# Optimization experiments

Measured on AMD Instinct MI355X. Metric: run time of the kernel, lower is better.

Reference implementation:

```python
import jax, jax.numpy as jnp
import numpy as np

EMBED_DIM = 1024
NUM_HEADS = 16
HEAD_DIM = EMBED_DIM // NUM_HEADS
B, S = 4, 2048


def setup_inputs() -> dict:
    key = jax.random.key(0)
    k1, k2, k3 = jax.random.split(key, 3)
    scale = 1.0 / np.sqrt(EMBED_DIM)
    x = jax.random.normal(k1, (B, S, EMBED_DIM), dtype=jnp.float32)
    W_qkv = jax.random.normal(k2, (EMBED_DIM, 3 * EMBED_DIM), dtype=jnp.float32) * scale
    b_qkv = jnp.zeros((3 * EMBED_DIM,), dtype=jnp.float32)
    W_out = jax.random.normal(k3, (EMBED_DIM, EMBED_DIM), dtype=jnp.float32) * scale
    b_out = jnp.zeros((EMBED_DIM,), dtype=jnp.float32)
    return {"x": x, "W_qkv": W_qkv, "b_qkv": b_qkv, "W_out": W_out, "b_out": b_out}


def reference(x, W_qkv, b_qkv, W_out, b_out):
    b, s, e = x.shape
    # fused QKV projection -> [b, s, 3, h, d]
    qkv = (x @ W_qkv + b_qkv).reshape(b, s, 3, NUM_HEADS, HEAD_DIM)
    qkv = jnp.transpose(qkv, (2, 0, 3, 1, 4))  # [3, b, h, s, d]
    q, k, v = qkv[0], qkv[1], qkv[2]
    scale = HEAD_DIM ** 0.5
    scores = jnp.einsum('bhqd,bhkd->bhqk', q, k) / scale  # [b, h, s, s]
    weights = jax.nn.softmax(scores, axis=-1)
    ctx = jnp.einsum('bhqk,bhkd->bhqd', weights, v)  # [b, h, s, d]
    ctx = jnp.transpose(ctx, (0, 2, 1, 3)).reshape(b, s, e)
    return ctx @ W_out + b_out
```

## Files before the change

### kernel.cpp

```cpp
#include <hip/hip_runtime.h>
#include <math.h>

#define B_ 4
#define S_ 2048
#define E_ 1024
#define H_ 16
#define D_ 64
#define M_TOT 8192
#define N_QKV 3072
#define K_ 1024

typedef __attribute__((ext_vector_type(8))) __bf16 bf16x8;
typedef __attribute__((ext_vector_type(2))) __bf16 bf16x2;
typedef __attribute__((ext_vector_type(8))) unsigned short u16x8;
typedef __attribute__((ext_vector_type(16))) float f32x16;

static __device__ __forceinline__ float bf2f(unsigned short u) {
  union { unsigned int u; float f; } x; x.u = ((unsigned int)u) << 16;
  return x.f;
}
static __device__ __forceinline__ unsigned int pack_bf16(float lo, float hi) {
  bf16x2 t; t[0] = (__bf16)lo; t[1] = (__bf16)hi;
  return __builtin_bit_cast(unsigned int, t);
}
static __device__ __forceinline__ void perm32swap(unsigned int& a, unsigned int& b) {
  asm volatile("v_permlane32_swap_b32 %0, %1" : "+v"(a), "+v"(b));
}

static __device__ __forceinline__ void gload16(const void* g, void* l) {
  __builtin_amdgcn_global_load_lds(
      (const __attribute__((address_space(1))) void*)g,
      (__attribute__((address_space(3))) void*)l, 16, 0, 0);
}

__global__ __launch_bounds__(256) void cvt_k(const float* __restrict__ in,
                                             unsigned short* __restrict__ out,
                                             int n8) {
  int i = blockIdx.x * 256 + threadIdx.x;
  if (i >= n8) return;
  float4 a = *reinterpret_cast<const float4*>(in + (size_t)i * 8);
  float4 b = *reinterpret_cast<const float4*>(in + (size_t)i * 8 + 4);
  uint4 o;
  o.x = pack_bf16(a.x, a.y); o.y = pack_bf16(a.z, a.w);
  o.z = pack_bf16(b.x, b.y); o.w = pack_bf16(b.z, b.w);
  *reinterpret_cast<uint4*>(out + (size_t)i * 8) = o;
}

__global__ __launch_bounds__(256) void tcvt_k(const float* __restrict__ in,
                                              unsigned short* __restrict__ out,
                                              int K, int N) {
  __shared__ float t[64][65];
  int n0 = blockIdx.x * 64, k0 = blockIdx.y * 64;
  int r = threadIdx.x >> 4, c = (threadIdx.x & 15) * 4;
#pragma unroll
  for (int it = 0; it < 4; ++it) {
    float4 v = *reinterpret_cast<const float4*>(&in[(size_t)(k0 + r + it * 16) * N + n0 + c]);
    t[r + it * 16][c + 0] = v.x; t[r + it * 16][c + 1] = v.y;
    t[r + it * 16][c + 2] = v.z; t[r + it * 16][c + 3] = v.w;
  }
  __syncthreads();
#pragma unroll
  for (int it = 0; it < 4; ++it) {
    int rr = r + it * 16;
    uint2 o;
    o.x = pack_bf16(t[c + 0][rr], t[c + 1][rr]);
    o.y = pack_bf16(t[c + 2][rr], t[c + 3][rr]);
    *reinterpret_cast<uint2*>(&out[(size_t)(n0 + rr) * K + k0 + c]) = o;
  }
}

template <int MODE>
__global__ __launch_bounds__(256) void gemm_k(
    const unsigned short* __restrict__ A, const unsigned short* __restrict__ BT,
    const float* __restrict__ bias, void* __restrict__ Cout,
    unsigned short* __restrict__ vT) {
  __shared__ __attribute__((aligned(128))) char lds[2][24576];
  const int tid = threadIdx.x;
  const int wv = tid >> 6, lane = tid & 63;
  const int ln = lane & 31, hh = lane >> 5;
  const int m0 = blockIdx.y * 128, n0 = blockIdx.x * 256;
  const int r4 = lane >> 2, slot = lane & 3;

  const char* Ab = (const char*)A;
  const char* Bb = (const char*)BT;
  size_t a_off[2], b_off[4];
#pragma unroll
  for (int i = 0; i < 2; ++i) {
    int r = wv * 32 + i * 16 + r4;
    a_off[i] = (size_t)(m0 + r) * (K_ * 2) + (size_t)((slot ^ ((r >> 1) & 3)) * 16);
  }
#pragma unroll
  for (int j = 0; j < 4; ++j) {
    int r = wv * 64 + j * 16 + r4;
    b_off[j] = (size_t)(n0 + r) * (K_ * 2) + (size_t)((slot ^ ((r >> 1) & 3)) * 16);
  }

  f32x16 acc[4][2];
#pragma unroll
  for (int gr = 0; gr < 4; ++gr)
#pragma unroll
    for (int gc = 0; gc < 2; ++gc)
#pragma unroll
      for (int e = 0; e < 16; ++e) acc[gr][gc][e] = 0.f;

#define STAGE(dst, tt)                                                        \
  do {                                                                        \
    char* _d = (dst);                                                         \
    size_t _ko = (size_t)(tt) * 64;                                           \
    _Pragma("unroll") for (int i = 0; i < 2; ++i)                             \
        gload16(Ab + a_off[i] + _ko, _d + (wv * 32 + i * 16) * 64);           \
    _Pragma("unroll") for (int j = 0; j < 4; ++j)                             \
        gload16(Bb + b_off[j] + _ko, _d + 8192 + (wv * 64 + j * 16) * 64);    \
  } while (0)

  STAGE(&lds[0][0], 0);
  __syncthreads();
  for (int t = 0; t < K_ / 32; ++t) {
    char* cur = &lds[t & 1][0];
    char* nxt = &lds[(t + 1) & 1][0];
    if (t + 1 < K_ / 32) STAGE(nxt, t + 1);
#pragma unroll
    for (int s = 0; s < 2; ++s) {
      const int cb = s * 32 + hh * 16;
      bf16x8 af[4], bfr[2];
#pragma unroll
      for (int gr = 0; gr < 4; ++gr) {
        int row = gr * 32 + ln;
        af[gr] = *reinterpret_cast<const bf16x8*>(
            cur + row * 64 + (cb ^ (((row >> 1) & 3) << 4)));
      }
#pragma unroll
      for (int gc = 0; gc < 2; ++gc) {
        int row = wv * 64 + gc * 32 + ln;
        bfr[gc] = *reinterpret_cast<const bf16x8*>(
            cur + 8192 + row * 64 + (cb ^ (((row >> 1) & 3) << 4)));
      }
#pragma unroll
      for (int gr = 0; gr < 4; ++gr)
#pragma unroll
        for (int gc = 0; gc < 2; ++gc)
          acc[gr][gc] = __builtin_amdgcn_mfma_f32_32x32x16_bf16(
              af[gr], bfr[gc], acc[gr][gc], 0, 0, 0);
    }
    __syncthreads();
  }
#undef STAGE

  const int ncol0 = n0 + wv * 64;
  if (MODE == 0) {
    unsigned short* qkv = (unsigned short*)Cout;
#pragma unroll
    for (int gc = 0; gc < 2; ++gc) {
      int n = ncol0 + gc * 32 + ln;
      float bv = bias[n];
      int which = n >> 10, h = (n >> 6) & 15, d = n & 63;
      if (which < 2) {
        unsigned short* base =
            qkv + (((size_t)which * B_ * H_ + h) * S_) * D_ + d;
#pragma unroll
        for (int gr = 0; gr < 4; ++gr)
#pragma unroll
          for (int r = 0; r < 16; r += 2) {
            int m = m0 + gr * 32 + 4 * hh + (r & 3) + 8 * (r >> 2);
            unsigned int w = pack_bf16(acc[gr][gc][r] + bv, acc[gr][gc][r + 1] + bv);
            int bi = m >> 11, si = m & 2047;
            size_t off = ((size_t)bi * H_ * S_ + si) * D_;
            base[off] = (unsigned short)w;
            base[off + D_] = (unsigned short)(w >> 16);
          }
      } else {
        unsigned short* vbase = vT + ((size_t)h * D_ + d) * S_;
#pragma unroll
        for (int gr = 0; gr < 4; ++gr)
#pragma unroll
          for (int rq = 0; rq < 4; ++rq) {
            int mb = m0 + gr * 32 + 4 * hh + 8 * rq;
            int bi = mb >> 11, si = mb & 2047;
            uint2 w;
            w.x = pack_bf16(acc[gr][gc][rq * 4 + 0] + bv, acc[gr][gc][rq * 4 + 1] + bv);
            w.y = pack_bf16(acc[gr][gc][rq * 4 + 2] + bv, acc[gr][gc][rq * 4 + 3] + bv);
            *reinterpret_cast<uint2*>(vbase + (size_t)bi * H_ * D_ * S_ + si) = w;
          }
      }
    }
  } else {
    float* out = (float*)Cout;
#pragma unroll
    for (int gc = 0; gc < 2; ++gc) {
      int n = ncol0 + gc * 32 + ln;
      float bv = bias[n];
#pragma unroll
      for (int gr = 0; gr < 4; ++gr)
#pragma unroll
        for (int r = 0; r < 16; ++r) {
          int m = m0 + gr * 32 + 4 * hh + (r & 3) + 8 * (r >> 2);
          out[(size_t)m * E_ + n] = acc[gr][gc][r] + bv;
        }
    }
  }
}

__global__ __launch_bounds__(256, 4) void attn_k(
    const unsigned short* __restrict__ qkv, const unsigned short* __restrict__ vT,
    unsigned short* __restrict__ ctx) {
  __shared__ __attribute__((aligned(128))) char lds[2][8192];
  const int tid = threadIdx.x;
  const int wv = tid >> 6;
  const int lane = tid & 63;
  const int ln = lane & 31;
  const int hh = lane >> 5;
  const int q0 = blockIdx.x * 128;
  const int bh = blockIdx.y;
  const int b = bh >> 4, head = bh & 15;
  const size_t SZ = (size_t)B_ * H_ * S_ * D_;
  const size_t plane = ((size_t)b * H_ + head) * (size_t)S_ * D_;
  const unsigned short* Qp = qkv + plane;
  const unsigned short* Kp = qkv + SZ + plane;
  const unsigned short* Vp = vT + ((size_t)b * H_ + head) * (size_t)D_ * S_;

  const float SC = 0.125f * 1.4426950408889634f;
  const int qrow = q0 + wv * 32 + ln;
  bf16x8 qf[4];
#pragma unroll
  for (int db = 0; db < 4; ++db) {
    u16x8 qr = *reinterpret_cast<const u16x8*>(Qp + (size_t)qrow * D_ + db * 16 + hh * 8);
    bf16x8 qs;
#pragma unroll
    for (int j = 0; j < 8; ++j) qs[j] = (__bf16)(bf2f(qr[j]) * SC);
    qf[db] = qs;
  }

  const size_t ksrc = (size_t)(tid >> 3) * 64 +
                      (size_t)(((tid & 7) ^ ((tid >> 3) & 7)) * 8);
  const size_t vsrc = (size_t)(tid >> 2) * S_ +
                      (size_t)(((tid & 3) ^ ((tid >> 3) & 3)) * 8);

#define ASTAGE(bsel, tt)                                                      \
  do {                                                                        \
    char* _d = &lds[(bsel)][0];                                               \
    gload16(Kp + (size_t)(tt) * 2048 + ksrc, _d + tid * 16);                  \
    gload16(Vp + (size_t)(tt) * 32 + vsrc, _d + 4096 + tid * 16);             \
  } while (0)

  ASTAGE(0, 0);
  __syncthreads();

  f32x16 acc0, acc1;
#pragma unroll
  for (int e = 0; e < 16; ++e) { acc0[e] = 0.f; acc1[e] = 0.f; }
  float mrun = 0.f, lrun = 0.f;
  const int xo = (ln >> 1) & 3;

  for (int t = 0; t < 64; ++t) {
    const int cb = t & 1;
    if (t + 1 < 64) ASTAGE(cb ^ 1, t + 1);
    const char* cur = &lds[cb][0];
    f32x16 st;
    const float nm = -mrun;
#pragma unroll
    for (int e = 0; e < 16; ++e) st[e] = nm;
    __builtin_amdgcn_s_setprio(1);
#pragma unroll
    for (int db = 0; db < 4; ++db) {
      bf16x8 kf = *reinterpret_cast<const bf16x8*>(
          cur + ln * 128 + ((((db << 1) | hh) ^ (ln & 7)) << 4));
      st = __builtin_amdgcn_mfma_f32_32x32x16_bf16(kf, qf[db], st, 0, 0, 0);
    }
    __builtin_amdgcn_s_setprio(0);
    const char* vb_ = cur + 4096;
    bf16x8 vA = *reinterpret_cast<const bf16x8*>(vb_ + ln * 64 + ((hh ^ xo) << 4));
    bf16x8 vB = *reinterpret_cast<const bf16x8*>(vb_ + ln * 64 + (((2 + hh) ^ xo) << 4));
    bf16x8 vC = *reinterpret_cast<const bf16x8*>(vb_ + (ln + 32) * 64 + ((hh ^ xo) << 4));
    bf16x8 vD = *reinterpret_cast<const bf16x8*>(vb_ + (ln + 32) * 64 + (((2 + hh) ^ xo) << 4));
    float m1 = fmaxf(fmaxf(st[0], st[1]), st[2]);
    float m2 = fmaxf(fmaxf(st[3], st[4]), st[5]);
    float m3 = fmaxf(fmaxf(st[6], st[7]), st[8]);
    float m4 = fmaxf(fmaxf(st[9], st[10]), st[11]);
    float m5 = fmaxf(fmaxf(st[12], st[13]), st[14]);
    float tm = fmaxf(fmaxf(fmaxf(m1, m2), fmaxf(m3, m4)), fmaxf(m5, st[15]));
    tm = fmaxf(tm, __shfl_xor(tm, 32, 64));
    if (!__all(tm <= 8.0f)) {
      float d = fmaxf(tm, 0.f);
      float alpha = __builtin_amdgcn_exp2f(-d);
      mrun += d;
      lrun *= alpha;
      acc0 *= alpha;
      acc1 *= alpha;
#pragma unroll
      for (int r = 0; r < 16; ++r) st[r] -= d;
    }
    float p[16];
#pragma unroll
    for (int r = 0; r < 16; ++r) p[r] = __builtin_amdgcn_exp2f(st[r]);
    float s0 = (p[0] + p[1]) + (p[2] + p[3]);
    float s1 = (p[4] + p[5]) + (p[6] + p[7]);
    float s2 = (p[8] + p[9]) + (p[10] + p[11]);
    float s3 = (p[12] + p[13]) + (p[14] + p[15]);
    float psum = (s0 + s1) + (s2 + s3);
    psum += __shfl_xor(psum, 32, 64);
    lrun += psum;
    unsigned int w0 = pack_bf16(p[0], p[1]);
    unsigned int w1 = pack_bf16(p[2], p[3]);
    unsigned int w2 = pack_bf16(p[4], p[5]);
    unsigned int w3 = pack_bf16(p[6], p[7]);
    unsigned int w4 = pack_bf16(p[8], p[9]);
    unsigned int w5 = pack_bf16(p[10], p[11]);
    unsigned int w6 = pack_bf16(p[12], p[13]);
    unsigned int w7 = pack_bf16(p[14], p[15]);
    perm32swap(w0, w2);
    perm32swap(w1, w3);
    perm32swap(w4, w6);
    perm32swap(w5, w7);
    bf16x8 pb0 = __builtin_bit_cast(bf16x8, make_uint4(w0, w1, w2, w3));
    bf16x8 pb1 = __builtin_bit_cast(bf16x8, make_uint4(w4, w5, w6, w7));
    __builtin_amdgcn_s_setprio(1);
    acc0 = __builtin_amdgcn_mfma_f32_32x32x16_bf16(vA, pb0, acc0, 0, 0, 0);
    acc0 = __builtin_amdgcn_mfma_f32_32x32x16_bf16(vB, pb1, acc0, 0, 0, 0);
    acc1 = __builtin_amdgcn_mfma_f32_32x32x16_bf16(vC, pb0, acc1, 0, 0, 0);
    acc1 = __builtin_amdgcn_mfma_f32_32x32x16_bf16(vD, pb1, acc1, 0, 0, 0);
    __builtin_amdgcn_s_setprio(0);
    __syncthreads();
  }
#undef ASTAGE

  float invl = 1.0f / lrun;
  unsigned short* orow = ctx + ((size_t)b * S_ + qrow) * E_ + head * D_;
#pragma unroll
  for (int g = 0; g < 4; ++g) {
    int d0 = 8 * g + 4 * hh;
    uint2 o0, o1;
    o0.x = pack_bf16(acc0[4 * g + 0] * invl, acc0[4 * g + 1] * invl);
    o0.y = pack_bf16(acc0[4 * g + 2] * invl, acc0[4 * g + 3] * invl);
    o1.x = pack_bf16(acc1[4 * g + 0] * invl, acc1[4 * g + 1] * invl);
    o1.y = pack_bf16(acc1[4 * g + 2] * invl, acc1[4 * g + 3] * invl);
    *reinterpret_cast<uint2*>(orow + d0) = o0;
    *reinterpret_cast<uint2*>(orow + d0 + 32) = o1;
  }
}

extern "C" void kernel_launch(void* const* d_in, const int* in_sizes, int n_in,
                              void* d_out, int out_size, void* d_ws, size_t ws_size,
                              hipStream_t stream) {
  const float* x    = (const float*)d_in[0];
  const float* Wqkv = (const float*)d_in[1];
  const float* bqkv = (const float*)d_in[2];
  const float* Wout = (const float*)d_in[3];
  const float* bout = (const float*)d_in[4];
  float* out = (float*)d_out;

  char* ws = (char*)d_ws;
  unsigned short* qkv_b = (unsigned short*)ws;  ws += (size_t)2 * B_ * H_ * S_ * D_ * 2;
  unsigned short* vT_b  = (unsigned short*)ws;  ws += (size_t)B_ * H_ * D_ * S_ * 2;
  unsigned short* ctx_b = (unsigned short*)ws;  ws += (size_t)M_TOT * E_ * 2;
  unsigned short* xb    = (unsigned short*)ws;  ws += (size_t)M_TOT * E_ * 2;
  unsigned short* wqT   = (unsigned short*)ws;  ws += (size_t)N_QKV * K_ * 2;
  unsigned short* woT   = (unsigned short*)ws;

  cvt_k<<<dim3(M_TOT * E_ / 8 / 256), 256, 0, stream>>>(x, xb, M_TOT * E_ / 8);
  tcvt_k<<<dim3(N_QKV / 64, K_ / 64), 256, 0, stream>>>(Wqkv, wqT, K_, N_QKV);
  tcvt_k<<<dim3(E_ / 64, K_ / 64), 256, 0, stream>>>(Wout, woT, K_, E_);

  gemm_k<0><<<dim3(N_QKV / 256, M_TOT / 128), 256, 0, stream>>>(xb, wqT, bqkv, qkv_b, vT_b);
  attn_k<<<dim3(S_ / 128, B_ * H_), 256, 0, stream>>>(qkv_b, vT_b, ctx_b);
  gemm_k<1><<<dim3(E_ / 256, M_TOT / 128), 256, 0, stream>>>(ctx_b, woT, bout, out, nullptr);
}
```

Before: 225.2 us.

## Load K/V fragments directly from global into registers, dropping LDS staging

The attention kernel no longer stages K and V tiles through double-buffered shared memory. Each wave now loads its own MFMA fragments straight from global memory into registers, prefetching the next tile during the current iteration, and the per-iteration block barrier is removed. This cuts LDS traffic and synchronisation, but the four waves of a block each fetch the same K/V data separately, so the kernel depends on L1/L2 to absorb the repeated global loads. The prefetch of the next tile also wraps around on the last iteration, which is a harmless extra load.

```diff
diff --git a/kernel.cpp b/kernel.cpp
--- a/kernel.cpp
+++ b/kernel.cpp
@@ -203,7 +203,6 @@
 __global__ __launch_bounds__(256, 4) void attn_k(
     const unsigned short* __restrict__ qkv, const unsigned short* __restrict__ vT,
     unsigned short* __restrict__ ctx) {
-  __shared__ __attribute__((aligned(128))) char lds[2][8192];
   const int tid = threadIdx.x;
   const int wv = tid >> 6;
   const int lane = tid & 63;
@@ -230,48 +229,40 @@
     qf[db] = qs;
   }
 
-  const size_t ksrc = (size_t)(tid >> 3) * 64 +
-                      (size_t)(((tid & 7) ^ ((tid >> 3) & 7)) * 8);
-  const size_t vsrc = (size_t)(tid >> 2) * S_ +
-                      (size_t)(((tid & 3) ^ ((tid >> 3) & 3)) * 8);
-
-#define ASTAGE(bsel, tt)                                                      \
-  do {                                                                        \
-    char* _d = &lds[(bsel)][0];                                               \
-    gload16(Kp + (size_t)(tt) * 2048 + ksrc, _d + tid * 16);                  \
-    gload16(Vp + (size_t)(tt) * 32 + vsrc, _d + 4096 + tid * 16);             \
-  } while (0)
-
-  ASTAGE(0, 0);
-  __syncthreads();
+  const unsigned short* kbase = Kp + (size_t)ln * D_ + hh * 8;
+  const unsigned short* vbase = Vp + (size_t)ln * S_ + hh * 8;
+
+  u16x8 kr[4], vr0, vr1, vr2, vr3;
+#pragma unroll
+  for (int db = 0; db < 4; ++db)
+    kr[db] = *reinterpret_cast<const u16x8*>(kbase + db * 16);
+  vr0 = *reinterpret_cast<const u16x8*>(vbase);
+  vr1 = *reinterpret_cast<const u16x8*>(vbase + 16);
+  vr2 = *reinterpret_cast<const u16x8*>(vbase + 32 * S_);
+  vr3 = *reinterpret_cast<const u16x8*>(vbase + 32 * S_ + 16);
 
   f32x16 acc0, acc1;
 #pragma unroll
   for (int e = 0; e < 16; ++e) { acc0[e] = 0.f; acc1[e] = 0.f; }
   float mrun = 0.f, lrun = 0.f;
-  const int xo = (ln >> 1) & 3;
 
   for (int t = 0; t < 64; ++t) {
-    const int cb = t & 1;
-    if (t + 1 < 64) ASTAGE(cb ^ 1, t + 1);
-    const char* cur = &lds[cb][0];
     f32x16 st;
     const float nm = -mrun;
 #pragma unroll
     for (int e = 0; e < 16; ++e) st[e] = nm;
     __builtin_amdgcn_s_setprio(1);
 #pragma unroll
-    for (int db = 0; db < 4; ++db) {
-      bf16x8 kf = *reinterpret_cast<const bf16x8*>(
-          cur + ln * 128 + ((((db << 1) | hh) ^ (ln & 7)) << 4));
-      st = __builtin_amdgcn_mfma_f32_32x32x16_bf16(kf, qf[db], st, 0, 0, 0);
-    }
+    for (int db = 0; db < 4; ++db)
+      st = __builtin_amdgcn_mfma_f32_32x32x16_bf16(
+          __builtin_bit_cast(bf16x8, kr[db]), qf[db], st, 0, 0, 0);
     __builtin_amdgcn_s_setprio(0);
-    const char* vb_ = cur + 4096;
-    bf16x8 vA = *reinterpret_cast<const bf16x8*>(vb_ + ln * 64 + ((hh ^ xo) << 4));
-    bf16x8 vB = *reinterpret_cast<const bf16x8*>(vb_ + ln * 64 + (((2 + hh) ^ xo) << 4));
-    bf16x8 vC = *reinterpret_cast<const bf16x8*>(vb_ + (ln + 32) * 64 + ((hh ^ xo) << 4));
-    bf16x8 vD = *reinterpret_cast<const bf16x8*>(vb_ + (ln + 32) * 64 + (((2 + hh) ^ xo) << 4));
+    {
+      const unsigned short* kb = kbase + (size_t)((t + 1) & 63) * 32 * D_;
+#pragma unroll
+      for (int db = 0; db < 4; ++db)
+        kr[db] = *reinterpret_cast<const u16x8*>(kb + db * 16);
+    }
     float m1 = fmaxf(fmaxf(st[0], st[1]), st[2]);
     float m2 = fmaxf(fmaxf(st[3], st[4]), st[5]);
     float m3 = fmaxf(fmaxf(st[6], st[7]), st[8]);
@@ -314,14 +305,23 @@
     bf16x8 pb0 = __builtin_bit_cast(bf16x8, make_uint4(w0, w1, w2, w3));
     bf16x8 pb1 = __builtin_bit_cast(bf16x8, make_uint4(w4, w5, w6, w7));
     __builtin_amdgcn_s_setprio(1);
-    acc0 = __builtin_amdgcn_mfma_f32_32x32x16_bf16(vA, pb0, acc0, 0, 0, 0);
-    acc0 = __builtin_amdgcn_mfma_f32_32x32x16_bf16(vB, pb1, acc0, 0, 0, 0);
-    acc1 = __builtin_amdgcn_mfma_f32_32x32x16_bf16(vC, pb0, acc1, 0, 0, 0);
-    acc1 = __builtin_amdgcn_mfma_f32_32x32x16_bf16(vD, pb1, acc1, 0, 0, 0);
+    acc0 = __builtin_amdgcn_mfma_f32_32x32x16_bf16(
+        __builtin_bit_cast(bf16x8, vr0), pb0, acc0, 0, 0, 0);
+    acc0 = __builtin_amdgcn_mfma_f32_32x32x16_bf16(
+        __builtin_bit_cast(bf16x8, vr1), pb1, acc0, 0, 0, 0);
+    acc1 = __builtin_amdgcn_mfma_f32_32x32x16_bf16(
+        __builtin_bit_cast(bf16x8, vr2), pb0, acc1, 0, 0, 0);
+    acc1 = __builtin_amdgcn_mfma_f32_32x32x16_bf16(
+        __builtin_bit_cast(bf16x8, vr3), pb1, acc1, 0, 0, 0);
     __builtin_amdgcn_s_setprio(0);
-    __syncthreads();
-  }
-#undef ASTAGE
+    {
+      const unsigned short* vb = vbase + ((t + 1) & 63) * 32;
+      vr0 = *reinterpret_cast<const u16x8*>(vb);
+      vr1 = *reinterpret_cast<const u16x8*>(vb + 16);
+      vr2 = *reinterpret_cast<const u16x8*>(vb + 32 * S_);
+      vr3 = *reinterpret_cast<const u16x8*>(vb + 32 * S_ + 16);
+    }
+  }
 
   float invl = 1.0f / lrun;
   unsigned short* orow = ctx + ((size_t)b * S_ + qrow) * E_ + head * D_;
```

New measurement: 358.1 us. 59.0% more time.
